# Optimization experiments

Measured on AMD Instinct MI355X. Metric: run time of the kernel, lower is better.

## Reference

```python
import jax, jax.numpy as jnp
import numpy as np

B, T, D, H = 4, 2048, 1024, 16
DH = D // H


def setup_inputs() -> dict:
    key = jax.random.key(0)
    ks = jax.random.split(key, 7)
    s = 1.0 / np.sqrt(D)
    inp = {
        "query": jax.random.normal(ks[0], (B, T, D), jnp.float32),
        "key": jax.random.normal(ks[1], (B, T, D), jnp.float32),
        "value": jax.random.normal(ks[2], (B, T, D), jnp.float32),
        "wq": jax.random.normal(ks[3], (D, D), jnp.float32) * s,
        "wk": jax.random.normal(ks[4], (D, D), jnp.float32) * s,
        "wv": jax.random.normal(ks[5], (D, D), jnp.float32) * s,
        "wo": jax.random.normal(ks[6], (D, D), jnp.float32) * s,
    }
    # additive causal mask, broadcast over batch and heads
    neg = jnp.finfo(jnp.float32).min
    causal = jnp.where(jnp.tril(jnp.ones((T, T), bool)), 0.0, neg)
    inp["attn_mask"] = causal[None, None, :, :].astype(jnp.float32)
    return inp


def _split_heads(x):
    # [B, T, D] -> [B, H, T, DH]
    Bx, Tx, _ = x.shape
    return x.reshape(Bx, Tx, H, DH).transpose(0, 2, 1, 3)


def reference(query, key, value, attn_mask, wq, wk, wv, wo):
    # nn.Linear(bias=False): y = x @ W^T
    q = _split_heads(query @ wq.T)
    k = _split_heads(key @ wk.T)
    v = _split_heads(value @ wv.T)
    scale = 1.0 / jnp.sqrt(jnp.asarray(DH, q.dtype))
    scores = jnp.einsum("bhqd,bhkd->bhqk", q, k) * scale + attn_mask
    weights = jax.nn.softmax(scores, axis=-1)
    out = jnp.einsum("bhqk,bhkd->bhqd", weights, v)
    out = out.transpose(0, 2, 1, 3).reshape(query.shape[0], query.shape[1], D)
    out = out @ wo.T
    return out, k, v
```

## Files before the change

kernel.cpp:

```cpp
#include <hip/hip_runtime.h>
#include <hip/hip_bf16.h>
#include <math.h>

constexpr int Mdim = 8192;
constexpr int Ndim = 1024;
constexpr int Kdim = 1024;
constexpr int Tseq = 2048;
constexpr int NH   = 16;

typedef __attribute__((ext_vector_type(8))) short short8;
typedef __attribute__((ext_vector_type(4))) float floatx4;

__device__ __forceinline__ unsigned short f2b(float f) {
  unsigned int x = __builtin_bit_cast(unsigned int, f);
  x += 0x7fffu + ((x >> 16) & 1u);
  return (unsigned short)(x >> 16);
}
__device__ __forceinline__ unsigned int pk2(float a, float b) {
  unsigned int ua = __builtin_bit_cast(unsigned int, a) + 0x8000u;
  unsigned int ub = __builtin_bit_cast(unsigned int, b) + 0x8000u;
  return (ua >> 16) | (ub & 0xffff0000u);
}
__device__ __forceinline__ void gld16(const void* g, const void* l) {
  __builtin_amdgcn_global_load_lds(
      (const __attribute__((address_space(1))) unsigned int*)(unsigned long long)g,
      (__attribute__((address_space(3))) unsigned int*)(unsigned int)(unsigned long long)l,
      16, 0, 0);
}

__global__ __launch_bounds__(256) void cast_k(
    const float* __restrict__ q, const float* __restrict__ k,
    const float* __restrict__ v, const float* __restrict__ wq,
    const float* __restrict__ wk, const float* __restrict__ wv,
    const float* __restrict__ wo,
    unsigned short* d0, unsigned short* d1, unsigned short* d2,
    unsigned short* d3, unsigned short* d4, unsigned short* d5,
    unsigned short* d6) {
  int y = blockIdx.y;
  const float* s = y == 0 ? q : y == 1 ? k : y == 2 ? v
                 : y == 3 ? wq : y == 4 ? wk : y == 5 ? wv : wo;
  unsigned short* d = y == 0 ? d0 : y == 1 ? d1 : y == 2 ? d2
                    : y == 3 ? d3 : y == 4 ? d4 : y == 5 ? d5 : d6;
  size_t n = (y < 3) ? (size_t)Mdim * Kdim : (size_t)Ndim * Kdim;
  size_t i = ((size_t)blockIdx.x * 256 + threadIdx.x) * 8;
  if (i >= n) return;
  float4 a = *(const float4*)(s + i);
  float4 b = *(const float4*)(s + i + 4);
  uint4 w;
  w.x = (unsigned)f2b(a.x) | ((unsigned)f2b(a.y) << 16);
  w.y = (unsigned)f2b(a.z) | ((unsigned)f2b(a.w) << 16);
  w.z = (unsigned)f2b(b.x) | ((unsigned)f2b(b.y) << 16);
  w.w = (unsigned)f2b(b.z) | ((unsigned)f2b(b.w) << 16);
  *(uint4*)(d + i) = w;
}

__launch_bounds__(256)
__global__ void gemm_qkv(const unsigned short* __restrict__ Aq,
                         const unsigned short* __restrict__ Ak,
                         const unsigned short* __restrict__ Av,
                         const unsigned short* __restrict__ Wq,
                         const unsigned short* __restrict__ Wk,
                         const unsigned short* __restrict__ Wv,
                         unsigned short* __restrict__ Qh,
                         unsigned short* __restrict__ Kh,
                         float* __restrict__ Kout,
                         unsigned short* __restrict__ VTg,
                         float* __restrict__ Vout) {
  __shared__ __align__(16) unsigned short As[128 * 32];
  __shared__ __align__(16) unsigned short Bs[128 * 32];

  const int z = blockIdx.z;
  const unsigned short* A = z == 0 ? Aq : z == 1 ? Ak : Av;
  const unsigned short* W = z == 0 ? Wq : z == 1 ? Wk : Wv;

  const int tid  = threadIdx.x;
  const int lane = tid & 63;
  const int wave = tid >> 6;
  const int l15  = lane & 15;
  const int quad = lane >> 4;
  const int m0 = blockIdx.y * 128;
  const int n0 = blockIdx.x * 128;
  const int wm = (wave >> 1) * 64;
  const int wn = (wave & 1) * 64;

  floatx4 acc[4][4];
  for (int i = 0; i < 4; i++)
    for (int j = 0; j < 4; j++) acc[i][j] = (floatx4)0.0f;

  const int c    = wave * 2;
  const int lrow = (lane >> 2);
  const int lcol = (lane & 3) * 8;

  for (int kt = 0; kt < Kdim; kt += 32) {
    for (int jj = 0; jj < 2; jj++) {
      int row = (c + jj) * 16 + lrow;
      gld16(A + (size_t)(m0 + row) * Kdim + kt + lcol, As + (c + jj) * 512);
      gld16(W + (size_t)(n0 + row) * Kdim + kt + lcol, Bs + (c + jj) * 512);
    }
    __syncthreads();

    short8 af[4], bfr[4];
    for (int mi = 0; mi < 4; mi++)
      af[mi] = *(const short8*)(As + (wm + mi * 16 + l15) * 32 + quad * 8);
    for (int ni = 0; ni < 4; ni++)
      bfr[ni] = *(const short8*)(Bs + (wn + ni * 16 + l15) * 32 + quad * 8);

    for (int mi = 0; mi < 4; mi++)
      for (int ni = 0; ni < 4; ni++)
        acc[mi][ni] = __builtin_amdgcn_mfma_f32_16x16x32_bf16(
            af[mi], bfr[ni], acc[mi][ni], 0, 0, 0);
    __syncthreads();
  }

  for (int mi = 0; mi < 4; mi++) {
    for (int ni = 0; ni < 4; ni++) {
      int gmb = m0 + wm + mi * 16 + quad * 4;
      int gn  = n0 + wn + ni * 16 + l15;
      int b = gmb >> 11, tb = gmb & (Tseq - 1);
      int h = gn >> 6, dh = gn & 63;
      size_t base = ((size_t)((b * NH + h) * Tseq + tb)) * 64 + dh;
      if (z == 0) {
        for (int r = 0; r < 4; r++) Qh[base + (size_t)r * 64] = f2b(acc[mi][ni][r]);
      } else if (z == 1) {
        for (int r = 0; r < 4; r++) {
          Kout[base + (size_t)r * 64] = acc[mi][ni][r];
          Kh[base + (size_t)r * 64] = f2b(acc[mi][ni][r]);
        }
      } else {
        ushort4 w;
        w.x = f2b(acc[mi][ni][0]); w.y = f2b(acc[mi][ni][1]);
        w.z = f2b(acc[mi][ni][2]); w.w = f2b(acc[mi][ni][3]);
        for (int r = 0; r < 4; r++) Vout[base + (size_t)r * 64] = acc[mi][ni][r];
        size_t vt = ((size_t)((b * NH + h) * 64 + dh)) * Tseq + tb;
        *(ushort4*)(VTg + vt) = w;
      }
    }
  }
}

__launch_bounds__(256)
__global__ void gemm_o(const unsigned short* __restrict__ A,
                       const unsigned short* __restrict__ W,
                       float* __restrict__ Cf) {
  __shared__ __align__(16) unsigned short As[128 * 32];
  __shared__ __align__(16) unsigned short Bs[128 * 32];

  const int tid  = threadIdx.x;
  const int lane = tid & 63;
  const int wave = tid >> 6;
  const int l15  = lane & 15;
  const int quad = lane >> 4;
  const int m0 = blockIdx.y * 128;
  const int n0 = blockIdx.x * 128;
  const int wm = (wave >> 1) * 64;
  const int wn = (wave & 1) * 64;

  floatx4 acc[4][4];
  for (int i = 0; i < 4; i++)
    for (int j = 0; j < 4; j++) acc[i][j] = (floatx4)0.0f;

  const int c    = wave * 2;
  const int lrow = (lane >> 2);
  const int lcol = (lane & 3) * 8;

  for (int kt = 0; kt < Kdim; kt += 32) {
    for (int jj = 0; jj < 2; jj++) {
      int row = (c + jj) * 16 + lrow;
      gld16(A + (size_t)(m0 + row) * Kdim + kt + lcol, As + (c + jj) * 512);
      gld16(W + (size_t)(n0 + row) * Kdim + kt + lcol, Bs + (c + jj) * 512);
    }
    __syncthreads();

    short8 af[4], bfr[4];
    for (int mi = 0; mi < 4; mi++)
      af[mi] = *(const short8*)(As + (wm + mi * 16 + l15) * 32 + quad * 8);
    for (int ni = 0; ni < 4; ni++)
      bfr[ni] = *(const short8*)(Bs + (wn + ni * 16 + l15) * 32 + quad * 8);

    for (int mi = 0; mi < 4; mi++)
      for (int ni = 0; ni < 4; ni++)
        acc[mi][ni] = __builtin_amdgcn_mfma_f32_16x16x32_bf16(
            af[mi], bfr[ni], acc[mi][ni], 0, 0, 0);
    __syncthreads();
  }

  for (int mi = 0; mi < 4; mi++)
    for (int ni = 0; ni < 4; ni++) {
      int gmb = m0 + wm + mi * 16 + quad * 4;
      int gn  = n0 + wn + ni * 16 + l15;
      for (int r = 0; r < 4; r++)
        Cf[(size_t)(gmb + r) * Ndim + gn] = acc[mi][ni][r];
    }
}

__launch_bounds__(256)
__global__ void attn_k(const unsigned short* __restrict__ Qh,
                       const unsigned short* __restrict__ Kh,
                       const unsigned short* __restrict__ VTg,
                       unsigned short* __restrict__ Og) {
  __shared__ __align__(16) unsigned short Kt[64 * 64];
  __shared__ __align__(16) unsigned short Vt[64 * 64];
  __shared__ __align__(16) unsigned short Pl[128 * 64];

  const int tid  = threadIdx.x;
  const int lane = tid & 63;
  const int wave = tid >> 6;
  const int l15  = lane & 15;
  const int quad = lane >> 4;
  const int sw   = l15 & 7;
  const int bh = blockIdx.x;
  const int qt = 15 - blockIdx.y;

  const size_t headoff = (size_t)bh * Tseq * 64;
  const int qbase = qt * 128 + wave * 32;

  short8 bq[2][2];
  for (int m = 0; m < 2; m++)
    for (int hf = 0; hf < 2; hf++)
      bq[m][hf] = *(const short8*)(Qh + headoff +
                                   (size_t)(qbase + m * 16 + l15) * 64 + hf * 32 + quad * 8);

  floatx4 o[2][4];
  for (int m = 0; m < 2; m++)
    for (int nb = 0; nb < 4; nb++) o[m][nb] = (floatx4)0.0f;
  float mrow[2] = {-INFINITY, -INFINITY};
  float lrow[2] = {0.0f, 0.0f};

  const int srow8 = lane >> 3;
  const int sg    = lane & 7;
  const int nkt   = 2 * qt + 2;
  const float kscale = 0.18033688011112042f;

  for (int kt = 0; kt < nkt; kt++) {
    const int k0 = kt * 64;
    for (int jj = 0; jj < 2; jj++) {
      int cc = wave * 2 + jj;
      int row = cc * 8 + srow8;
      int G = sg ^ (row & 7);
      gld16(Kh + headoff + (size_t)(k0 + row) * 64 + G * 8, Kt + cc * 512);
      gld16(VTg + ((size_t)bh * 64 + row) * Tseq + k0 + G * 8, Vt + cc * 512);
    }
    __syncthreads();

    floatx4 st[2][4];
    for (int nb = 0; nb < 4; nb++) {
      const unsigned short* kr = Kt + (nb * 16 + l15) * 64;
      short8 ak0 = *(const short8*)(kr + ((quad ^ sw) << 3));
      short8 ak1 = *(const short8*)(kr + (((quad + 4) ^ sw) << 3));
      for (int m = 0; m < 2; m++) {
        floatx4 a = (floatx4)0.0f;
        a = __builtin_amdgcn_mfma_f32_16x16x32_bf16(ak0, bq[m][0], a, 0, 0, 0);
        a = __builtin_amdgcn_mfma_f32_16x16x32_bf16(ak1, bq[m][1], a, 0, 0, 0);
        st[m][nb] = a;
      }
    }

    if (k0 + 63 > qbase) {
      for (int m = 0; m < 2; m++) {
        int qg = qbase + m * 16 + l15;
        for (int nb = 0; nb < 4; nb++)
          for (int r = 0; r < 4; r++) {
            int kg = k0 + nb * 16 + quad * 4 + r;
            if (kg > qg) st[m][nb][r] = -INFINITY;
          }
      }
    }

    for (int m = 0; m < 2; m++) {
      float mt = fmaxf(fmaxf(st[m][0][0], st[m][0][1]), fmaxf(st[m][0][2], st[m][0][3]));
      for (int nb = 1; nb < 4; nb++)
        mt = fmaxf(mt, fmaxf(fmaxf(st[m][nb][0], st[m][nb][1]),
                             fmaxf(st[m][nb][2], st[m][nb][3])));
      mt = fmaxf(mt, __shfl_xor(mt, 16, 64));
      mt = fmaxf(mt, __shfl_xor(mt, 32, 64));
      float mnew = fmaxf(mrow[m], mt);
      float al = __builtin_amdgcn_exp2f((mrow[m] - mnew) * kscale);
      mrow[m] = mnew;
      const float ms = mnew * kscale;

      float rs = 0.0f;
      const int prow = (wave * 32 + m * 16 + l15) * 64;
      for (int nb = 0; nb < 4; nb++) {
        float p0 = __builtin_amdgcn_exp2f(__builtin_fmaf(st[m][nb][0], kscale, -ms));
        float p1 = __builtin_amdgcn_exp2f(__builtin_fmaf(st[m][nb][1], kscale, -ms));
        float p2 = __builtin_amdgcn_exp2f(__builtin_fmaf(st[m][nb][2], kscale, -ms));
        float p3 = __builtin_amdgcn_exp2f(__builtin_fmaf(st[m][nb][3], kscale, -ms));
        rs += (p0 + p1) + (p2 + p3);
        uint2 w = {pk2(p0, p1), pk2(p2, p3)};
        int klb = nb * 16 + quad * 4;
        int colp = (((klb >> 3) ^ sw) << 3) | (klb & 7);
        *(uint2*)(Pl + prow + colp) = w;
      }
      rs += __shfl_xor(rs, 16, 64);
      rs += __shfl_xor(rs, 32, 64);
      lrow[m] = lrow[m] * al + rs;
      for (int nb = 0; nb < 4; nb++)
        for (int r = 0; r < 4; r++) o[m][nb][r] *= al;
    }

    short8 av[4][2];
    for (int nb = 0; nb < 4; nb++) {
      const unsigned short* vr = Vt + (nb * 16 + l15) * 64;
      av[nb][0] = *(const short8*)(vr + ((quad ^ sw) << 3));
      av[nb][1] = *(const short8*)(vr + (((quad + 4) ^ sw) << 3));
    }
    for (int m = 0; m < 2; m++) {
      const unsigned short* pr = Pl + (wave * 32 + m * 16 + l15) * 64;
      short8 bp0 = *(const short8*)(pr + ((quad ^ sw) << 3));
      short8 bp1 = *(const short8*)(pr + (((quad + 4) ^ sw) << 3));
      for (int nb = 0; nb < 4; nb++) {
        o[m][nb] = __builtin_amdgcn_mfma_f32_16x16x32_bf16(av[nb][0], bp0, o[m][nb], 0, 0, 0);
        o[m][nb] = __builtin_amdgcn_mfma_f32_16x16x32_bf16(av[nb][1], bp1, o[m][nb], 0, 0, 0);
      }
    }
    __syncthreads();
  }

  const int b = bh >> 4, h = bh & 15;
  for (int m = 0; m < 2; m++) {
    float inv = 1.0f / lrow[m];
    int q = qbase + m * 16 + l15;
    size_t rowoff = ((size_t)(b * Tseq + q)) * 1024 + h * 64;
    for (int nb = 0; nb < 4; nb++) {
      ushort4 w;
      w.x = f2b(o[m][nb][0] * inv);
      w.y = f2b(o[m][nb][1] * inv);
      w.z = f2b(o[m][nb][2] * inv);
      w.w = f2b(o[m][nb][3] * inv);
      *(ushort4*)(Og + rowoff + nb * 16 + quad * 4) = w;
    }
  }
}

extern "C" void kernel_launch(void* const* d_in, const int* in_sizes, int n_in,
                              void* d_out, int out_size, void* d_ws, size_t ws_size,
                              hipStream_t stream) {
  const float* q  = (const float*)d_in[0];
  const float* k  = (const float*)d_in[1];
  const float* v  = (const float*)d_in[2];
  const float* wq = (const float*)d_in[3];
  const float* wk = (const float*)d_in[4];
  const float* wv = (const float*)d_in[5];
  const float* wo = (const float*)d_in[6];
  float* out = (float*)d_out;

  constexpr size_t BTD = (size_t)Mdim * Kdim;
  constexpr size_t DD  = (size_t)Ndim * Kdim;
  constexpr size_t MB16 = BTD * 2;

  char* ws = (char*)d_ws;
  unsigned short* Qh  = (unsigned short*)(ws);
  unsigned short* Kh  = (unsigned short*)(ws + MB16);
  unsigned short* VTg = (unsigned short*)(ws + 2 * MB16);
  unsigned short* Og  = (unsigned short*)(ws + 3 * MB16);
  unsigned short* qb  = (unsigned short*)(ws + 4 * MB16);
  unsigned short* kb  = (unsigned short*)(ws + 5 * MB16);
  unsigned short* vb  = (unsigned short*)(ws + 6 * MB16);
  unsigned short* wqb = (unsigned short*)(ws + 7 * MB16);
  unsigned short* wkb = wqb + DD;
  unsigned short* wvb = wkb + DD;
  unsigned short* wob = wvb + DD;

  float* Kout = out + BTD;
  float* Vout = out + 2 * BTD;

  cast_k<<<dim3(4096, 7), 256, 0, stream>>>(q, k, v, wq, wk, wv, wo,
                                            qb, kb, vb, wqb, wkb, wvb, wob);

  gemm_qkv<<<dim3(Ndim / 128, Mdim / 128, 3), 256, 0, stream>>>(
      qb, kb, vb, wqb, wkb, wvb, Qh, Kh, Kout, VTg, Vout);

  attn_k<<<dim3(4 * NH, Tseq / 128), 256, 0, stream>>>(Qh, Kh, VTg, Og);

  gemm_o<<<dim3(Ndim / 128, Mdim / 128), 256, 0, stream>>>(Og, wob, out);
}
```

Baseline: 396.2 us.

## Widen GEMM K-tile to 64 with XOR-swizzled LDS and transposed MFMA output

Both projection GEMMs now stage a 64-wide K slice per iteration instead of 32, halving the number of barrier pairs per K loop. The LDS layout is XOR-swizzled by row to avoid bank conflicts on the 16-byte fragment reads. MFMA operands are swapped so each lane holds four consecutive N columns, which allows vectorized float4/ushort4 stores for Q, K, V and the output. The trade-off is that the V-transpose store becomes four scalar stores, and LDS use doubles, which may reduce occupancy.

```diff
diff --git a/kernel.cpp b/kernel.cpp
--- a/kernel.cpp
+++ b/kernel.cpp
@@ -66,8 +66,8 @@
                          float* __restrict__ Kout,
                          unsigned short* __restrict__ VTg,
                          float* __restrict__ Vout) {
-  __shared__ __align__(16) unsigned short As[128 * 32];
-  __shared__ __align__(16) unsigned short Bs[128 * 32];
+  __shared__ __align__(16) unsigned short As[128 * 64];
+  __shared__ __align__(16) unsigned short Bs[128 * 64];
 
   const int z = blockIdx.z;
   const unsigned short* A = z == 0 ? Aq : z == 1 ? Ak : Av;
@@ -78,6 +78,7 @@
   const int wave = tid >> 6;
   const int l15  = lane & 15;
   const int quad = lane >> 4;
+  const int sw   = l15 & 7;
   const int m0 = blockIdx.y * 128;
   const int n0 = blockIdx.x * 128;
   const int wm = (wave >> 1) * 64;
@@ -87,52 +88,56 @@
   for (int i = 0; i < 4; i++)
     for (int j = 0; j < 4; j++) acc[i][j] = (floatx4)0.0f;
 
-  const int c    = wave * 2;
-  const int lrow = (lane >> 2);
-  const int lcol = (lane & 3) * 8;
-
-  for (int kt = 0; kt < Kdim; kt += 32) {
-    for (int jj = 0; jj < 2; jj++) {
-      int row = (c + jj) * 16 + lrow;
-      gld16(A + (size_t)(m0 + row) * Kdim + kt + lcol, As + (c + jj) * 512);
-      gld16(W + (size_t)(n0 + row) * Kdim + kt + lcol, Bs + (c + jj) * 512);
-    }
-    __syncthreads();
-
-    short8 af[4], bfr[4];
-    for (int mi = 0; mi < 4; mi++)
-      af[mi] = *(const short8*)(As + (wm + mi * 16 + l15) * 32 + quad * 8);
-    for (int ni = 0; ni < 4; ni++)
-      bfr[ni] = *(const short8*)(Bs + (wn + ni * 16 + l15) * 32 + quad * 8);
-
-    for (int mi = 0; mi < 4; mi++)
+  const int srow8 = lane >> 3;
+  const int sg    = lane & 7;
+
+  for (int kt = 0; kt < Kdim; kt += 64) {
+    for (int jj = 0; jj < 4; jj++) {
+      int cc = wave * 4 + jj;
+      int row = cc * 8 + srow8;
+      int G = sg ^ (row & 7);
+      gld16(A + (size_t)(m0 + row) * Kdim + kt + G * 8, As + cc * 512);
+      gld16(W + (size_t)(n0 + row) * Kdim + kt + G * 8, Bs + cc * 512);
+    }
+    __syncthreads();
+
+    for (int hf = 0; hf < 2; hf++) {
+      short8 af[4], bw[4];
+      for (int mi = 0; mi < 4; mi++)
+        af[mi] = *(const short8*)(As + (wm + mi * 16 + l15) * 64 +
+                                  (((hf * 4 + quad) ^ sw) << 3));
       for (int ni = 0; ni < 4; ni++)
-        acc[mi][ni] = __builtin_amdgcn_mfma_f32_16x16x32_bf16(
-            af[mi], bfr[ni], acc[mi][ni], 0, 0, 0);
-    __syncthreads();
-  }
-
+        bw[ni] = *(const short8*)(Bs + (wn + ni * 16 + l15) * 64 +
+                                  (((hf * 4 + quad) ^ sw) << 3));
+      for (int mi = 0; mi < 4; mi++)
+        for (int ni = 0; ni < 4; ni++)
+          acc[mi][ni] = __builtin_amdgcn_mfma_f32_16x16x32_bf16(
+              bw[ni], af[mi], acc[mi][ni], 0, 0, 0);
+    }
+    __syncthreads();
+  }
+
+  const int gm = m0 + wm + l15;
   for (int mi = 0; mi < 4; mi++) {
+    int t_abs = gm + mi * 16;
+    int b = t_abs >> 11, tb = t_abs & (Tseq - 1);
     for (int ni = 0; ni < 4; ni++) {
-      int gmb = m0 + wm + mi * 16 + quad * 4;
-      int gn  = n0 + wn + ni * 16 + l15;
-      int b = gmb >> 11, tb = gmb & (Tseq - 1);
-      int h = gn >> 6, dh = gn & 63;
-      size_t base = ((size_t)((b * NH + h) * Tseq + tb)) * 64 + dh;
+      int gn0 = n0 + wn + ni * 16 + quad * 4;
+      int h = gn0 >> 6, dh0 = gn0 & 63;
+      size_t base = ((size_t)((b * NH + h) * Tseq + tb)) * 64 + dh0;
+      floatx4 v = acc[mi][ni];
       if (z == 0) {
-        for (int r = 0; r < 4; r++) Qh[base + (size_t)r * 64] = f2b(acc[mi][ni][r]);
+        ushort4 w = {f2b(v[0]), f2b(v[1]), f2b(v[2]), f2b(v[3])};
+        *(ushort4*)(Qh + base) = w;
       } else if (z == 1) {
-        for (int r = 0; r < 4; r++) {
-          Kout[base + (size_t)r * 64] = acc[mi][ni][r];
-          Kh[base + (size_t)r * 64] = f2b(acc[mi][ni][r]);
-        }
+        *(float4*)(Kout + base) = *(float4*)&v;
+        ushort4 w = {f2b(v[0]), f2b(v[1]), f2b(v[2]), f2b(v[3])};
+        *(ushort4*)(Kh + base) = w;
       } else {
-        ushort4 w;
-        w.x = f2b(acc[mi][ni][0]); w.y = f2b(acc[mi][ni][1]);
-        w.z = f2b(acc[mi][ni][2]); w.w = f2b(acc[mi][ni][3]);
-        for (int r = 0; r < 4; r++) Vout[base + (size_t)r * 64] = acc[mi][ni][r];
-        size_t vt = ((size_t)((b * NH + h) * 64 + dh)) * Tseq + tb;
-        *(ushort4*)(VTg + vt) = w;
+        *(float4*)(Vout + base) = *(float4*)&v;
+        size_t vtb = ((size_t)((b * NH + h) * 64 + dh0)) * Tseq + tb;
+        for (int r = 0; r < 4; r++)
+          VTg[vtb + (size_t)r * Tseq] = f2b(v[r]);
       }
     }
   }
@@ -142,14 +147,15 @@
 __global__ void gemm_o(const unsigned short* __restrict__ A,
                        const unsigned short* __restrict__ W,
                        float* __restrict__ Cf) {
-  __shared__ __align__(16) unsigned short As[128 * 32];
-  __shared__ __align__(16) unsigned short Bs[128 * 32];
+  __shared__ __align__(16) unsigned short As[128 * 64];
+  __shared__ __align__(16) unsigned short Bs[128 * 64];
 
   const int tid  = threadIdx.x;
   const int lane = tid & 63;
   const int wave = tid >> 6;
   const int l15  = lane & 15;
   const int quad = lane >> 4;
+  const int sw   = l15 & 7;
   const int m0 = blockIdx.y * 128;
   const int n0 = blockIdx.x * 128;
   const int wm = (wave >> 1) * 64;
@@ -159,38 +165,43 @@
   for (int i = 0; i < 4; i++)
     for (int j = 0; j < 4; j++) acc[i][j] = (floatx4)0.0f;
 
-  const int c    = wave * 2;
-  const int lrow = (lane >> 2);
-  const int lcol = (lane & 3) * 8;
-
-  for (int kt = 0; kt < Kdim; kt += 32) {
-    for (int jj = 0; jj < 2; jj++) {
-      int row = (c + jj) * 16 + lrow;
-      gld16(A + (size_t)(m0 + row) * Kdim + kt + lcol, As + (c + jj) * 512);
-      gld16(W + (size_t)(n0 + row) * Kdim + kt + lcol, Bs + (c + jj) * 512);
-    }
-    __syncthreads();
-
-    short8 af[4], bfr[4];
-    for (int mi = 0; mi < 4; mi++)
-      af[mi] = *(const short8*)(As + (wm + mi * 16 + l15) * 32 + quad * 8);
-    for (int ni = 0; ni < 4; ni++)
-      bfr[ni] = *(const short8*)(Bs + (wn + ni * 16 + l15) * 32 + quad * 8);
-
-    for (int mi = 0; mi < 4; mi++)
+  const int srow8 = lane >> 3;
+  const int sg    = lane & 7;
+
+  for (int kt = 0; kt < Kdim; kt += 64) {
+    for (int jj = 0; jj < 4; jj++) {
+      int cc = wave * 4 + jj;
+      int row = cc * 8 + srow8;
+      int G = sg ^ (row & 7);
+      gld16(A + (size_t)(m0 + row) * Kdim + kt + G * 8, As + cc * 512);
+      gld16(W + (size_t)(n0 + row) * Kdim + kt + G * 8, Bs + cc * 512);
+    }
+    __syncthreads();
+
+    for (int hf = 0; hf < 2; hf++) {
+      short8 af[4], bw[4];
+      for (int mi = 0; mi < 4; mi++)
+        af[mi] = *(const short8*)(As + (wm + mi * 16 + l15) * 64 +
+                                  (((hf * 4 + quad) ^ sw) << 3));
       for (int ni = 0; ni < 4; ni++)
-        acc[mi][ni] = __builtin_amdgcn_mfma_f32_16x16x32_bf16(
-            af[mi], bfr[ni], acc[mi][ni], 0, 0, 0);
-    __syncthreads();
-  }
-
-  for (int mi = 0; mi < 4; mi++)
+        bw[ni] = *(const short8*)(Bs + (wn + ni * 16 + l15) * 64 +
+                                  (((hf * 4 + quad) ^ sw) << 3));
+      for (int mi = 0; mi < 4; mi++)
+        for (int ni = 0; ni < 4; ni++)
+          acc[mi][ni] = __builtin_amdgcn_mfma_f32_16x16x32_bf16(
+              bw[ni], af[mi], acc[mi][ni], 0, 0, 0);
+    }
+    __syncthreads();
+  }
+
+  for (int mi = 0; mi < 4; mi++) {
+    int t_abs = m0 + wm + mi * 16 + l15;
     for (int ni = 0; ni < 4; ni++) {
-      int gmb = m0 + wm + mi * 16 + quad * 4;
-      int gn  = n0 + wn + ni * 16 + l15;
-      for (int r = 0; r < 4; r++)
-        Cf[(size_t)(gmb + r) * Ndim + gn] = acc[mi][ni][r];
-    }
+      int gn0 = n0 + wn + ni * 16 + quad * 4;
+      floatx4 v = acc[mi][ni];
+      *(float4*)(Cf + (size_t)t_abs * Ndim + gn0) = *(float4*)&v;
+    }
+  }
 }
 
 __launch_bounds__(256)
```

After: 381.7 us. -3.7%, faster.
